# Performance work log

Measured on AMD Instinct MI355X. Metric: run time of the kernel, lower is better.

## Reference

```python
import jax, jax.numpy as jnp
import numpy as np

N_NODES = 50000
N_EDGES = 800000
NFEAT = 128
NHID = 128
NCLASS = 10
NUM_GRAPHS = 512


def setup_inputs() -> dict:
    key = jax.random.key(0)
    ks = jax.random.split(key, 8)
    node_feat = jax.random.normal(ks[0], (N_NODES, NFEAT), dtype=jnp.float32)
    W1 = jax.random.normal(ks[1], (NFEAT, NHID), dtype=jnp.float32) * (1.0 / np.sqrt(NFEAT))
    W2 = jax.random.normal(ks[2], (NHID, NHID), dtype=jnp.float32) * (1.0 / np.sqrt(NHID))
    mlp_w = jax.random.normal(ks[3], (NHID, NCLASS), dtype=jnp.float32) * (1.0 / np.sqrt(NHID))
    mlp_b = jnp.zeros((NCLASS,), dtype=jnp.float32)
    edge_src = jax.random.randint(ks[4], (N_EDGES,), 0, N_NODES, dtype=jnp.int32)
    edge_dst = jax.random.randint(ks[5], (N_EDGES,), 0, N_NODES, dtype=jnp.int32)
    graph_ids = jnp.sort(jax.random.randint(ks[6], (N_NODES,), 0, NUM_GRAPHS, dtype=jnp.int32))
    return {"node_feat": node_feat, "W1": W1, "W2": W2, "mlp_w": mlp_w,
            "mlp_b": mlp_b, "edge_src": edge_src, "edge_dst": edge_dst,
            "graph_ids": graph_ids}


def reference(node_feat, W1, W2, mlp_w, mlp_b, edge_src, edge_dst, graph_ids):
    # node_degs: in-degree + 1 (self loop), as used by GraphConvolution's normalization
    ones_e = jnp.ones((N_EDGES,), dtype=node_feat.dtype)
    deg = jax.ops.segment_sum(ones_e, edge_dst, num_segments=N_NODES) + 1.0  # [N]

    def gconv(x, W):
        h = x @ W                                                     # [N, H]
        msg = jax.ops.segment_sum(h[edge_src], edge_dst, num_segments=N_NODES)
        return (h + msg) / deg[:, None]                               # mean over self + neighbors

    x = jax.nn.relu(gconv(node_feat, W1))
    x = gconv(x, W2)                                                  # [N, NHID]

    # per-graph mean readout (the Python loop over graph_sizes == segment mean)
    counts = jax.ops.segment_sum(jnp.ones((N_NODES,), x.dtype), graph_ids,
                                 num_segments=NUM_GRAPHS)             # [G]
    gsum = jax.ops.segment_sum(x, graph_ids, num_segments=NUM_GRAPHS)  # [G, NHID]
    gmean = gsum / jnp.maximum(counts, 1.0)[:, None]

    logits = gmean @ mlp_w + mlp_b                                    # [G, NCLASS]
    return jax.nn.log_softmax(logits, axis=1)
```

## Files before the change

kernel.cpp:

```cpp
#include <hip/hip_runtime.h>

#define N_NODES 50000
#define N_EDGES 800000
#define NFEAT 128
#define NHID 128
#define NCLASS 10
#define NUM_GRAPHS 512
#define GEMM_BLOCKS 391
#define SLOT 64
#define NBUK 391
#define ECAP 512
#define CPAD 32

typedef __attribute__((ext_vector_type(8))) short bf16x8;
typedef __attribute__((ext_vector_type(4))) float f32x4;

__device__ inline ushort f2bf(float f) {
  union { float f; uint u; } c; c.f = f;
  return (ushort)((c.u + 0x7fffu + ((c.u >> 16) & 1u)) >> 16);
}
__device__ inline float bf2f_lo(uint u) { union { uint u; float f; } c; c.u = u << 16; return c.f; }
__device__ inline float bf2f_hi(uint u) { union { uint u; float f; } c; c.u = u & 0xffff0000u; return c.f; }

template <bool RELU>
__device__ inline void gemm_body(const ushort* __restrict__ Xv,
                                 const ushort* __restrict__ Wp,
                                 ushort* __restrict__ Y,
                                 ushort* xs, ushort* wsh,
                                 int base, int tid) {
  const int rem = N_NODES - base;
  for (int i = tid; i < 2048; i += 512)
    ((uint4*)wsh)[i] = ((const uint4*)Wp)[i];

  for (int g = tid; g < 2048; g += 512) {
    int row = g >> 4;
    int k0 = (g & 15) << 3;
    int wt = row >> 4, ks = k0 >> 5;
    int lane = (row & 15) + (((k0 >> 3) & 3) << 4);
    uint4 v;
    if (row < rem) {
      v = *(const uint4*)(Xv + (size_t)(base + row) * 128 + k0);
    } else {
      v.x = 0; v.y = 0; v.z = 0; v.w = 0;
    }
    *(uint4*)&xs[((((wt << 2) + ks) << 6) + lane) << 3] = v;
  }
  __syncthreads();

  const int wave = tid >> 6, lane = tid & 63;
  f32x4 acc[8];
#pragma unroll
  for (int i = 0; i < 8; ++i) acc[i] = f32x4{0.f, 0.f, 0.f, 0.f};
  bf16x8 a[4];
#pragma unroll
  for (int ks = 0; ks < 4; ++ks)
    a[ks] = *(const bf16x8*)&xs[((((wave << 2) + ks) << 6) + lane) << 3];
#pragma unroll
  for (int ks = 0; ks < 4; ++ks) {
#pragma unroll
    for (int nt = 0; nt < 8; ++nt) {
      bf16x8 b = *(const bf16x8*)&wsh[((((nt << 2) + ks) << 6) + lane) << 3];
      acc[nt] = __builtin_amdgcn_mfma_f32_16x16x32_bf16(a[ks], b, acc[nt], 0, 0, 0);
    }
  }
  const int r0 = base + wave * 16 + ((lane >> 4) << 2);
  const int c0 = lane & 15;
#pragma unroll
  for (int nt = 0; nt < 8; ++nt)
#pragma unroll
    for (int r = 0; r < 4; ++r) {
      int row = r0 + r;
      if (row < N_NODES) {
        float v = acc[nt][r];
        if (RELU) v = fmaxf(v, 0.f);
        Y[(size_t)row * 128 + (nt << 4) + c0] = f2bf(v);
      }
    }
}

__global__ __launch_bounds__(512) void k_gemm1(const ushort* __restrict__ X,
                                               const ushort* __restrict__ Wp,
                                               ushort* __restrict__ Y) {
  __shared__ ushort xs[8 * 4 * 64 * 8];
  __shared__ ushort wsh[32 * 64 * 8];
  gemm_body<true>(X, Wp, Y, xs, wsh, blockIdx.x * 128, threadIdx.x);
}

__global__ __launch_bounds__(256) void k_wpack(const float* __restrict__ W,
                                               ushort* __restrict__ op) {
  int j = blockIdx.x * 256 + threadIdx.x;
  int lane = (j >> 3) & 63;
  int e = j & 7;
  int frag = j >> 9;
  int nt = frag >> 2, ks = frag & 3;
  int c = nt * 16 + (lane & 15);
  int k = ks * 32 + (lane >> 4) * 8 + e;
  op[j] = f2bf(W[k * 128 + c]);
}

__global__ __launch_bounds__(256) void k_cvt(const float* __restrict__ f,
                                             ushort* __restrict__ o) {
  int i = blockIdx.x * 256 + threadIdx.x;
  float4 v = ((const float4*)f)[i];
  uint2 p;
  p.x = (uint)f2bf(v.x) | ((uint)f2bf(v.y) << 16);
  p.y = (uint)f2bf(v.z) | ((uint)f2bf(v.w) << 16);
  ((uint2*)o)[i] = p;
}

__global__ __launch_bounds__(256) void k_scat(const int* __restrict__ esrc,
                                              const int* __restrict__ edst,
                                              int* __restrict__ cnt8,
                                              uint* __restrict__ ebuf) {
  uint xcc;
  asm volatile("s_getreg_b32 %0, hwreg(HW_REG_XCC_ID)" : "=s"(xcc));
  const int x = (int)(xcc & 7);
  for (int e = blockIdx.x * 256 + threadIdx.x; e < N_EDGES; e += gridDim.x * 256) {
    int d = edst[e];
    int bk = d >> 7;
    int dloc = d & 127;
    int p = atomicAdd(&cnt8[((bk << 3) + x) * CPAD], 1);
    if (p < ECAP)
      ebuf[(((size_t)bk << 3) + x) * ECAP + p] = (uint)esrc[e] | ((uint)dloc << 16);
  }
}

__global__ __launch_bounds__(256) void k_csr(const uint* __restrict__ ebuf,
                                             const int* __restrict__ cnt8,
                                             ushort* __restrict__ csr16,
                                             int* __restrict__ cnt) {
  __shared__ ushort csr_l[4096];
  __shared__ int cntL[128], off[128], cur[128];
  __shared__ int len8[8];
  const int b = blockIdx.x, tid = threadIdx.x;
  const int n0 = b << 7;
  const int nmax = min(128, N_NODES - n0);
  if (tid < 8) len8[tid] = min(cnt8[((b << 3) + tid) * CPAD], ECAP);
  for (int i = tid; i < 128; i += 256) { cntL[i] = 0; cur[i] = 0; }
  __syncthreads();
#pragma unroll
  for (int x = 0; x < 8; ++x) {
    const uint* s = ebuf + (((size_t)b << 3) + x) * ECAP;
    for (int i = tid; i < len8[x]; i += 256)
      atomicAdd(&cntL[s[i] >> 16], 1);
  }
  __syncthreads();
  if (tid == 0) {
    int o = 0;
    for (int n = 0; n < 128; ++n) { off[n] = o; o += min(cntL[n], SLOT); }
  }
  __syncthreads();
#pragma unroll
  for (int x = 0; x < 8; ++x) {
    const uint* s = ebuf + (((size_t)b << 3) + x) * ECAP;
    for (int i = tid; i < len8[x]; i += 256) {
      uint u = s[i];
      int dl = u >> 16;
      int p = atomicAdd(&cur[dl], 1);
      if (p < SLOT) csr_l[off[dl] + p] = (ushort)(u & 0xffffu);
    }
  }
  __syncthreads();
  for (int n = tid; n < nmax; n += 256) cnt[n0 + n] = min(cntL[n], SLOT);
  uint* outp = (uint*)csr16 + ((size_t)n0 << 5);
  const int tot = nmax << 5;
  for (int j = tid; j < tot; j += 256) {
    int n = j >> 5, k = (j & 31) << 1;
    int c = min(cntL[n], SLOT);
    uint lo = (k < c) ? (uint)csr_l[off[n] + k] : 0u;
    uint hi = (k + 1 < c) ? (uint)csr_l[off[n] + k + 1] : 0u;
    outp[((size_t)n << 5) + (j & 31)] = lo | (hi << 16);
  }
}

__device__ inline void unpack_add(uint4 u, float4& a0, float4& a1) {
  a0.x += bf2f_lo(u.x); a0.y += bf2f_hi(u.x);
  a0.z += bf2f_lo(u.y); a0.w += bf2f_hi(u.y);
  a1.x += bf2f_lo(u.z); a1.y += bf2f_hi(u.z);
  a1.z += bf2f_lo(u.w); a1.w += bf2f_hi(u.w);
}

__device__ inline void gather_sum(const uint4* __restrict__ Hv,
                                  const ushort* __restrict__ nb,
                                  int deg, int q, float4& a0, float4& a1) {
  int e = 0;
  for (; e + 8 <= deg; e += 8) {
    uint4 iv = *(const uint4*)(nb + e);
    uint4 u0 = Hv[(size_t)(iv.x & 0xffffu) * 16 + q];
    uint4 u1 = Hv[(size_t)(iv.x >> 16) * 16 + q];
    uint4 u2 = Hv[(size_t)(iv.y & 0xffffu) * 16 + q];
    uint4 u3 = Hv[(size_t)(iv.y >> 16) * 16 + q];
    uint4 u4 = Hv[(size_t)(iv.z & 0xffffu) * 16 + q];
    uint4 u5 = Hv[(size_t)(iv.z >> 16) * 16 + q];
    uint4 u6 = Hv[(size_t)(iv.w & 0xffffu) * 16 + q];
    uint4 u7 = Hv[(size_t)(iv.w >> 16) * 16 + q];
    unpack_add(u0, a0, a1); unpack_add(u1, a0, a1);
    unpack_add(u2, a0, a1); unpack_add(u3, a0, a1);
    unpack_add(u4, a0, a1); unpack_add(u5, a0, a1);
    unpack_add(u6, a0, a1); unpack_add(u7, a0, a1);
  }
  if (e + 4 <= deg) {
    uint2 iv = *(const uint2*)(nb + e);
    uint4 u0 = Hv[(size_t)(iv.x & 0xffffu) * 16 + q];
    uint4 u1 = Hv[(size_t)(iv.x >> 16) * 16 + q];
    uint4 u2 = Hv[(size_t)(iv.y & 0xffffu) * 16 + q];
    uint4 u3 = Hv[(size_t)(iv.y >> 16) * 16 + q];
    unpack_add(u0, a0, a1); unpack_add(u1, a0, a1);
    unpack_add(u2, a0, a1); unpack_add(u3, a0, a1);
    e += 4;
  }
  for (; e < deg; ++e) {
    uint4 u = Hv[(size_t)nb[e] * 16 + q];
    unpack_add(u, a0, a1);
  }
}

__global__ __launch_bounds__(256) void k_agg0(const ushort* __restrict__ H,
                                              const ushort* __restrict__ csr16,
                                              const int* __restrict__ cnt,
                                              ushort* __restrict__ Out) {
  const int q = threadIdx.x & 15;
  const int node = blockIdx.x * 16 + (threadIdx.x >> 4);
  const int deg = min(cnt[node], SLOT);
  const ushort* nb = csr16 + (size_t)node * SLOT;
  const uint4* __restrict__ Hv = (const uint4*)H;
  float4 a0 = {0.f, 0.f, 0.f, 0.f}, a1 = {0.f, 0.f, 0.f, 0.f};
  gather_sum(Hv, nb, deg, q, a0, a1);
  uint4 uh = Hv[(size_t)node * 16 + q];
  float inv = 1.0f / (float)(deg + 1);
  float v0 = (bf2f_lo(uh.x) + a0.x) * inv;
  float v1 = (bf2f_hi(uh.x) + a0.y) * inv;
  float v2 = (bf2f_lo(uh.y) + a0.z) * inv;
  float v3 = (bf2f_hi(uh.y) + a0.w) * inv;
  float v4 = (bf2f_lo(uh.z) + a1.x) * inv;
  float v5 = (bf2f_hi(uh.z) + a1.y) * inv;
  float v6 = (bf2f_lo(uh.w) + a1.z) * inv;
  float v7 = (bf2f_hi(uh.w) + a1.w) * inv;
  uint4 ov;
  ov.x = (uint)f2bf(v0) | ((uint)f2bf(v1) << 16);
  ov.y = (uint)f2bf(v2) | ((uint)f2bf(v3) << 16);
  ov.z = (uint)f2bf(v4) | ((uint)f2bf(v5) << 16);
  ov.w = (uint)f2bf(v6) | ((uint)f2bf(v7) << 16);
  ((uint4*)Out)[(size_t)node * 16 + q] = ov;
}

__global__ __launch_bounds__(256) void k_agg_ro(const ushort* __restrict__ H,
                                                const ushort* __restrict__ csr16,
                                                const int* __restrict__ cnt,
                                                const int* __restrict__ gid,
                                                float* __restrict__ gsum,
                                                float* __restrict__ gcnt) {
  __shared__ float rows[16][128];
  __shared__ int gids[16];
  const int q = threadIdx.x & 15;
  const int slot = threadIdx.x >> 4;
  const int node = blockIdx.x * 16 + slot;
  const int deg = min(cnt[node], SLOT);
  const ushort* nb = csr16 + (size_t)node * SLOT;
  const uint4* __restrict__ Hv = (const uint4*)H;
  float4 a0 = {0.f, 0.f, 0.f, 0.f}, a1 = {0.f, 0.f, 0.f, 0.f};
  gather_sum(Hv, nb, deg, q, a0, a1);
  uint4 uh = Hv[(size_t)node * 16 + q];
  float inv = 1.0f / (float)(deg + 1);
  float4 r0, r1;
  r0.x = (bf2f_lo(uh.x) + a0.x) * inv;
  r0.y = (bf2f_hi(uh.x) + a0.y) * inv;
  r0.z = (bf2f_lo(uh.y) + a0.z) * inv;
  r0.w = (bf2f_hi(uh.y) + a0.w) * inv;
  r1.x = (bf2f_lo(uh.z) + a1.x) * inv;
  r1.y = (bf2f_hi(uh.z) + a1.y) * inv;
  r1.z = (bf2f_lo(uh.w) + a1.z) * inv;
  r1.w = (bf2f_hi(uh.w) + a1.w) * inv;
  *(float4*)&rows[slot][q * 8] = r0;
  *(float4*)&rows[slot][q * 8 + 4] = r1;
  if (q == 0) gids[slot] = gid[node];
  __syncthreads();
  const int t = threadIdx.x;
  if (t < 128) {
    float acc = rows[0][t];
    int g = gids[0];
#pragma unroll
    for (int r = 1; r < 16; ++r) {
      int gr = gids[r];
      if (gr != g) {
        atomicAdd(&gsum[g * 128 + t], acc);
        acc = 0.f;
        g = gr;
      }
      acc += rows[r][t];
    }
    atomicAdd(&gsum[g * 128 + t], acc);
  } else if (t == 128) {
    float c = 1.f;
    int g = gids[0];
#pragma unroll
    for (int r = 1; r < 16; ++r) {
      int gr = gids[r];
      if (gr != g) {
        atomicAdd(&gcnt[g], c);
        c = 0.f;
        g = gr;
      }
      c += 1.f;
    }
    atomicAdd(&gcnt[g], c);
  }
}

__global__ __launch_bounds__(128) void k_mlp2(const float* __restrict__ gsum,
                                              const float* __restrict__ gcnt,
                                              const float* __restrict__ W2,
                                              const float* __restrict__ Wm,
                                              const float* __restrict__ bm,
                                              float* __restrict__ out) {
  __shared__ float m[128];
  __shared__ float h[128];
  __shared__ float lg[NCLASS];
  const int g = blockIdx.x;
  const int t = threadIdx.x;
  float c = fmaxf(gcnt[g], 1.0f);
  m[t] = gsum[g * 128 + t] / c;
  __syncthreads();
  float s = 0.f;
#pragma unroll
  for (int k = 0; k < 128; ++k) s += m[k] * W2[k * 128 + t];
  h[t] = s;
  __syncthreads();
  if (t < NCLASS) {
    float l = bm[t];
#pragma unroll
    for (int k = 0; k < 128; ++k) l += h[k] * Wm[k * NCLASS + t];
    lg[t] = l;
  }
  __syncthreads();
  if (t < NCLASS) {
    float mx = lg[0];
#pragma unroll
    for (int i = 1; i < NCLASS; ++i) mx = fmaxf(mx, lg[i]);
    float sum = 0.f;
#pragma unroll
    for (int i = 0; i < NCLASS; ++i) sum += expf(lg[i] - mx);
    out[g * NCLASS + t] = lg[t] - mx - logf(sum);
  }
}

extern "C" void kernel_launch(void* const* d_in, const int* in_sizes, int n_in,
                              void* d_out, int out_size, void* d_ws, size_t ws_size,
                              hipStream_t stream) {
  const float* feat = (const float*)d_in[0];
  const float* W1   = (const float*)d_in[1];
  const float* W2   = (const float*)d_in[2];
  const float* Wm   = (const float*)d_in[3];
  const float* bm   = (const float*)d_in[4];
  const int* esrc   = (const int*)d_in[5];
  const int* edst   = (const int*)d_in[6];
  const int* gid    = (const int*)d_in[7];
  float* out = (float*)d_out;

  int* cnt8     = (int*)d_ws;
  int* cnt      = cnt8 + NBUK * 8 * CPAD;
  uint* ebuf    = (uint*)(cnt + 50048);
  ushort* csr16 = (ushort*)(ebuf + (size_t)NBUK * 8 * ECAP);
  ushort* wp1   = csr16 + (size_t)50048 * SLOT;
  ushort* bufA  = wp1 + 16384;
  ushort* bufB  = bufA + (size_t)N_NODES * NHID;
  float* gsum   = (float*)(bufB + (size_t)N_NODES * NHID);
  float* gcnt   = gsum + NUM_GRAPHS * NHID;

  hipMemsetAsync(cnt8, 0, (size_t)NBUK * 8 * CPAD * sizeof(int), stream);
  hipMemsetAsync(gsum, 0, (size_t)(NUM_GRAPHS * NHID + 512) * sizeof(float), stream);

  k_wpack<<<64, 256, 0, stream>>>(W1, wp1);
  k_cvt<<<(N_NODES * NHID / 4 + 255) / 256, 256, 0, stream>>>(feat, bufA);
  k_scat<<<1024, 256, 0, stream>>>(esrc, edst, cnt8, ebuf);
  k_csr<<<NBUK, 256, 0, stream>>>(ebuf, cnt8, csr16, cnt);

  k_agg0<<<N_NODES / 16, 256, 0, stream>>>(bufA, csr16, cnt, bufB);
  k_gemm1<<<GEMM_BLOCKS, 512, 0, stream>>>(bufB, wp1, bufA);
  k_agg_ro<<<N_NODES / 16, 256, 0, stream>>>(bufA, csr16, cnt, gid, gsum, gcnt);
  k_mlp2<<<NUM_GRAPHS, 128, 0, stream>>>(gsum, gcnt, W2, Wm, bm, out);
}
```

Before: 225.6 us.

## Fuse prep kernels into one launch and bucket CSR neighbors by source range

Merges the weight-pack, feature-convert and edge-scatter kernels into a single k_prep launch dispatched by block index, removing two kernel launches and their serialization gaps. In k_csr, neighbor lists are now ordered by source chunk (src>>13) through per-node, per-chunk counting and prefix offsets, so later gathers read source rows with better locality. The cost is an extra shared-memory counting pass and more shared-memory atomics in the CSR build.

New measurement: 218.9 us. 2.9% less time.

```diff
diff --git a/kernel.cpp b/kernel.cpp
--- a/kernel.cpp
+++ b/kernel.cpp
@@ -12,6 +12,11 @@
 #define ECAP 512
 #define CPAD 32
 
+#define P_SCAT 1024
+#define P_WPACK 64
+#define P_CVT 6250
+#define P_GRID (P_SCAT + P_WPACK + P_CVT)
+
 typedef __attribute__((ext_vector_type(8))) short bf16x8;
 typedef __attribute__((ext_vector_type(4))) float f32x4;
 
@@ -86,42 +91,44 @@
   gemm_body<true>(X, Wp, Y, xs, wsh, blockIdx.x * 128, threadIdx.x);
 }
 
-__global__ __launch_bounds__(256) void k_wpack(const float* __restrict__ W,
-                                               ushort* __restrict__ op) {
-  int j = blockIdx.x * 256 + threadIdx.x;
-  int lane = (j >> 3) & 63;
-  int e = j & 7;
-  int frag = j >> 9;
-  int nt = frag >> 2, ks = frag & 3;
-  int c = nt * 16 + (lane & 15);
-  int k = ks * 32 + (lane >> 4) * 8 + e;
-  op[j] = f2bf(W[k * 128 + c]);
-}
-
-__global__ __launch_bounds__(256) void k_cvt(const float* __restrict__ f,
-                                             ushort* __restrict__ o) {
-  int i = blockIdx.x * 256 + threadIdx.x;
-  float4 v = ((const float4*)f)[i];
-  uint2 p;
-  p.x = (uint)f2bf(v.x) | ((uint)f2bf(v.y) << 16);
-  p.y = (uint)f2bf(v.z) | ((uint)f2bf(v.w) << 16);
-  ((uint2*)o)[i] = p;
-}
-
-__global__ __launch_bounds__(256) void k_scat(const int* __restrict__ esrc,
+__global__ __launch_bounds__(256) void k_prep(const int* __restrict__ esrc,
                                               const int* __restrict__ edst,
                                               int* __restrict__ cnt8,
-                                              uint* __restrict__ ebuf) {
-  uint xcc;
-  asm volatile("s_getreg_b32 %0, hwreg(HW_REG_XCC_ID)" : "=s"(xcc));
-  const int x = (int)(xcc & 7);
-  for (int e = blockIdx.x * 256 + threadIdx.x; e < N_EDGES; e += gridDim.x * 256) {
-    int d = edst[e];
-    int bk = d >> 7;
-    int dloc = d & 127;
-    int p = atomicAdd(&cnt8[((bk << 3) + x) * CPAD], 1);
-    if (p < ECAP)
-      ebuf[(((size_t)bk << 3) + x) * ECAP + p] = (uint)esrc[e] | ((uint)dloc << 16);
+                                              uint* __restrict__ ebuf,
+                                              const float* __restrict__ W1,
+                                              ushort* __restrict__ wp1,
+                                              const float* __restrict__ feat,
+                                              ushort* __restrict__ fb) {
+  const int b = blockIdx.x;
+  const int tid = threadIdx.x;
+  if (b < P_SCAT) {
+    uint xcc;
+    asm volatile("s_getreg_b32 %0, hwreg(HW_REG_XCC_ID)" : "=s"(xcc));
+    const int x = (int)(xcc & 7);
+    for (int e = b * 256 + tid; e < N_EDGES; e += P_SCAT * 256) {
+      int d = edst[e];
+      int bk = d >> 7;
+      int dloc = d & 127;
+      int p = atomicAdd(&cnt8[((bk << 3) + x) * CPAD], 1);
+      if (p < ECAP)
+        ebuf[(((size_t)bk << 3) + x) * ECAP + p] = (uint)esrc[e] | ((uint)dloc << 16);
+    }
+  } else if (b < P_SCAT + P_WPACK) {
+    int j = (b - P_SCAT) * 256 + tid;
+    int lane = (j >> 3) & 63;
+    int e = j & 7;
+    int frag = j >> 9;
+    int nt = frag >> 2, ks = frag & 3;
+    int c = nt * 16 + (lane & 15);
+    int k = ks * 32 + (lane >> 4) * 8 + e;
+    wp1[j] = f2bf(W1[k * 128 + c]);
+  } else {
+    int i = (b - P_SCAT - P_WPACK) * 256 + tid;
+    float4 v = ((const float4*)feat)[i];
+    uint2 p;
+    p.x = (uint)f2bf(v.x) | ((uint)f2bf(v.y) << 16);
+    p.y = (uint)f2bf(v.z) | ((uint)f2bf(v.w) << 16);
+    ((uint2*)fb)[i] = p;
   }
 }
 
@@ -130,25 +137,16 @@
                                              ushort* __restrict__ csr16,
                                              int* __restrict__ cnt) {
   __shared__ ushort csr_l[4096];
-  __shared__ int cntL[128], off[128], cur[128];
+  __shared__ int cntL[128], off[128];
+  __shared__ int cofs[128 * 8];
+  __shared__ int cur8[128 * 8];
   __shared__ int len8[8];
   const int b = blockIdx.x, tid = threadIdx.x;
   const int n0 = b << 7;
   const int nmax = min(128, N_NODES - n0);
   if (tid < 8) len8[tid] = min(cnt8[((b << 3) + tid) * CPAD], ECAP);
-  for (int i = tid; i < 128; i += 256) { cntL[i] = 0; cur[i] = 0; }
-  __syncthreads();
-#pragma unroll
-  for (int x = 0; x < 8; ++x) {
-    const uint* s = ebuf + (((size_t)b << 3) + x) * ECAP;
-    for (int i = tid; i < len8[x]; i += 256)
-      atomicAdd(&cntL[s[i] >> 16], 1);
-  }
-  __syncthreads();
-  if (tid == 0) {
-    int o = 0;
-    for (int n = 0; n < 128; ++n) { off[n] = o; o += min(cntL[n], SLOT); }
-  }
+  for (int i = tid; i < 128; i += 256) cntL[i] = 0;
+  for (int i = tid; i < 1024; i += 256) { cofs[i] = 0; cur8[i] = 0; }
   __syncthreads();
 #pragma unroll
   for (int x = 0; x < 8; ++x) {
@@ -156,8 +154,36 @@
     for (int i = tid; i < len8[x]; i += 256) {
       uint u = s[i];
       int dl = u >> 16;
-      int p = atomicAdd(&cur[dl], 1);
-      if (p < SLOT) csr_l[off[dl] + p] = (ushort)(u & 0xffffu);
+      int ck = (u & 0xffffu) >> 13;
+      atomicAdd(&cntL[dl], 1);
+      atomicAdd(&cofs[(dl << 3) + ck], 1);
+    }
+  }
+  __syncthreads();
+  if (tid == 0) {
+    int o = 0;
+    for (int n = 0; n < 128; ++n) { off[n] = o; o += min(cntL[n], SLOT); }
+  }
+  if (tid < 128) {
+    int s = 0;
+#pragma unroll
+    for (int k = 0; k < 8; ++k) {
+      int c = cofs[(tid << 3) + k];
+      cofs[(tid << 3) + k] = s;
+      s += c;
+    }
+  }
+  __syncthreads();
+#pragma unroll
+  for (int x = 0; x < 8; ++x) {
+    const uint* s = ebuf + (((size_t)b << 3) + x) * ECAP;
+    for (int i = tid; i < len8[x]; i += 256) {
+      uint u = s[i];
+      int dl = u >> 16;
+      int ck = (u & 0xffffu) >> 13;
+      int p = atomicAdd(&cur8[(dl << 3) + ck], 1);
+      int idx = cofs[(dl << 3) + ck] + p;
+      if (idx < SLOT) csr_l[off[dl] + idx] = (ushort)(u & 0xffffu);
     }
   }
   __syncthreads();
@@ -370,9 +396,7 @@
   hipMemsetAsync(cnt8, 0, (size_t)NBUK * 8 * CPAD * sizeof(int), stream);
   hipMemsetAsync(gsum, 0, (size_t)(NUM_GRAPHS * NHID + 512) * sizeof(float), stream);
 
-  k_wpack<<<64, 256, 0, stream>>>(W1, wp1);
-  k_cvt<<<(N_NODES * NHID / 4 + 255) / 256, 256, 0, stream>>>(feat, bufA);
-  k_scat<<<1024, 256, 0, stream>>>(esrc, edst, cnt8, ebuf);
+  k_prep<<<P_GRID, 256, 0, stream>>>(esrc, edst, cnt8, ebuf, W1, wp1, feat, bufA);
   k_csr<<<NBUK, 256, 0, stream>>>(ebuf, cnt8, csr16, cnt);
 
   k_agg0<<<N_NODES / 16, 256, 0, stream>>>(bufA, csr16, cnt, bufB);
```
